# Performance work log

Measured on AMD Instinct MI355X. Metric: run time of the kernel, lower is better.

## Reference

```python
import jax, jax.numpy as jnp
import numpy as np

B, S, H = 2, 2048, 1024
NH, HD = 16, 64
EPS = 1e-12
SCALE = float(np.sqrt(HD))


def layer_norm(x, g, b, eps=EPS):
    m = jnp.mean(x, axis=-1, keepdims=True)
    v = jnp.mean(jnp.square(x - m), axis=-1, keepdims=True)
    return (x - m) * jax.lax.rsqrt(v + eps) * g + b


def setup_inputs() -> dict:
    key = jax.random.key(0)
    ks = jax.random.split(key, 12)
    std = 0.02 / np.sqrt(2 * 24)  # num_hidden_layers = 24
    return {
        "hidden_states": jax.random.normal(ks[0], (B, S, H), dtype=jnp.float32),
        "attention_mask": jnp.ones((B, S), dtype=jnp.float32),
        "Wq": jax.random.normal(ks[1], (H, H), dtype=jnp.float32) * std,
        "bq": jnp.zeros((H,), dtype=jnp.float32),
        "Wk": jax.random.normal(ks[2], (H, H), dtype=jnp.float32) * std,
        "bk": jnp.zeros((H,), dtype=jnp.float32),
        "Wv": jax.random.normal(ks[3], (H, H), dtype=jnp.float32) * std,
        "bv": jnp.zeros((H,), dtype=jnp.float32),
        "Wd": jax.random.normal(ks[4], (H, H), dtype=jnp.float32) * (1.0 / np.sqrt(H)),
        "bd": jnp.zeros((H,), dtype=jnp.float32),
        "ln_g": jnp.ones((H,), dtype=jnp.float32),
        "ln_b": jnp.zeros((H,), dtype=jnp.float32),
    }


def reference(hidden_states, attention_mask, Wq, bq, Wk, bk, Wv, bv, Wd, bd, ln_g, ln_b):
    x = hidden_states
    # NOTE: source computes pre_attention_norm(x) but the no-cache path uses raw x for Q/K/V.
    def heads(t):  # [B,S,H] -> [B,NH,S,HD]
        return t.reshape(B, S, NH, HD).transpose(0, 2, 1, 3)

    q = heads(x @ Wq.T + bq)
    k = heads(x @ Wk.T + bk)
    v = heads(x @ Wv.T + bv)

    scores = jnp.einsum("bhqd,bhkd->bhqk", q, k) / SCALE
    mask = (1.0 - attention_mask) * -10000.0  # [B,S] -> broadcast [B,1,1,S]
    scores = scores + mask[:, None, None, :]
    probs = jax.nn.softmax(scores.astype(jnp.float32), axis=-1).astype(x.dtype)

    ctx = jnp.einsum("bhqk,bhkd->bhqd", probs, v)
    ctx = ctx.transpose(0, 2, 1, 3).reshape(B, S, NH * HD)

    out = ctx @ Wd.T + bd
    out = layer_norm(out + x, ln_g, ln_b)
    out = jnp.where(jnp.isfinite(out), out, jnp.zeros_like(out))
    return out
```

## Files before the change

### kernel.cpp

```cpp
#include <hip/hip_runtime.h>
#include <cstdint>
#include <cstddef>

#define B_    2
#define S_    2048
#define H_    1024
#define NH_   16
#define HD_   64

typedef __attribute__((ext_vector_type(8))) __bf16 bf16x8;
typedef __attribute__((ext_vector_type(4))) __bf16 bf16x4;
typedef __attribute__((ext_vector_type(4))) float  f32x4;

typedef __attribute__((address_space(1))) const unsigned int gcu32_t;
typedef __attribute__((address_space(3))) unsigned int lu32_t;
#define GLOAD16(gp, lp) __builtin_amdgcn_global_load_lds((gcu32_t*)(gp), (lu32_t*)(lp), 16, 0, 0)

#if __has_builtin(__builtin_amdgcn_exp2f)
#define EXP2F(x) __builtin_amdgcn_exp2f(x)
#else
#define EXP2F(x) exp2f(x)
#endif

__device__ __forceinline__ short f2bf(float f) {
  union { float f; unsigned u; } v; v.f = f;
  unsigned r = v.u + 0x7fffu + ((v.u >> 16) & 1u);
  return (short)(r >> 16);
}

__global__ __launch_bounds__(256) void convert_kernel(
    const float* __restrict__ x,  const float* __restrict__ wq,
    const float* __restrict__ wk, const float* __restrict__ wv,
    const float* __restrict__ wd,
    short* __restrict__ xb,  short* __restrict__ wqb, short* __restrict__ wkb,
    short* __restrict__ wvb, short* __restrict__ wdb) {
  size_t i = ((size_t)blockIdx.x * 256 + threadIdx.x) * 4;
  const float* src; short* dst; size_t off;
  if      (i < 4194304u) { src = x;  dst = xb;  off = i; }
  else if (i < 5242880u) { src = wq; dst = wqb; off = i - 4194304u; }
  else if (i < 6291456u) { src = wk; dst = wkb; off = i - 5242880u; }
  else if (i < 7340032u) { src = wv; dst = wvb; off = i - 6291456u; }
  else                   { src = wd; dst = wdb; off = i - 7340032u; }
  float4 v = *(const float4*)(src + off);
  short4 o; o.x = f2bf(v.x); o.y = f2bf(v.y); o.z = f2bf(v.z); o.w = f2bf(v.w);
  *(short4*)(dst + off) = o;
}

template<int MODE>
__global__ __launch_bounds__(256, 2) void gemm_bt(
    const short* __restrict__ A,
    const short* __restrict__ Bq, const short* __restrict__ Bk,
    const short* __restrict__ Bv,
    const float* __restrict__ biasq, const float* __restrict__ biask,
    const float* __restrict__ biasv,
    short* __restrict__ outq, short* __restrict__ outk, short* __restrict__ outv,
    float* __restrict__ outy) {
  __shared__ short As[128 * 64];
  __shared__ short Bs[128 * 64];

  const short* Bw; const float* bias; short* outs = nullptr;
  if (MODE == 0) {
    int z = blockIdx.z;
    Bw   = (z == 0) ? Bq    : ((z == 1) ? Bk    : Bv);
    bias = (z == 0) ? biasq : ((z == 1) ? biask : biasv);
    outs = (z == 0) ? outq  : ((z == 1) ? outk  : outv);
  } else {
    Bw = Bq; bias = biasq;
  }

  const int K = 1024;
  int tid  = threadIdx.x;
  int lane = tid & 63, w = tid >> 6;
  int wr = w >> 1, wc = w & 1;
  int m0 = blockIdx.y * 128, n0 = blockIdx.x * 128;
  int l15 = lane & 15, lg = lane >> 4;

  int lr = lane >> 3, lc8 = 8 * ((lane & 7) ^ lr);
  const short* Ag = A  + (size_t)(m0 + w * 8 + lr) * K + lc8;
  const short* Bg = Bw + (size_t)(n0 + w * 8 + lr) * K + lc8;

  int cxor = (l15 & 7) * 8;

  f32x4 acc[4][4];
  for (int m = 0; m < 4; m++)
    for (int n = 0; n < 4; n++) acc[m][n] = {0.f, 0.f, 0.f, 0.f};

  for (int kt = 0; kt < 16; kt++) {
    __syncthreads();
    for (int it = 0; it < 4; it++) {
      GLOAD16(Ag + (size_t)it * 32 * K + kt * 64, &As[(w * 8 + it * 32) * 64]);
      GLOAD16(Bg + (size_t)it * 32 * K + kt * 64, &Bs[(w * 8 + it * 32) * 64]);
    }
    __syncthreads();
#pragma unroll
    for (int kkh = 0; kkh < 2; kkh++) {
      int col = (kkh * 32 + lg * 8) ^ cxor;
      bf16x8 af[4], bfr[4];
#pragma unroll
      for (int m = 0; m < 4; m++)
        af[m] = *(const bf16x8*)&As[(wr * 64 + m * 16 + l15) * 64 + col];
#pragma unroll
      for (int n = 0; n < 4; n++)
        bfr[n] = *(const bf16x8*)&Bs[(wc * 64 + n * 16 + l15) * 64 + col];
#pragma unroll
      for (int m = 0; m < 4; m++)
#pragma unroll
        for (int n = 0; n < 4; n++)
          acc[m][n] = __builtin_amdgcn_mfma_f32_16x16x32_bf16(af[m], bfr[n], acc[m][n], 0, 0, 0);
    }
  }

  for (int n = 0; n < 4; n++) {
    int col = n0 + wc * 64 + n * 16 + l15;
    float bval = bias[col];
    if (MODE == 0) {
      int h = col >> 6, d = col & 63;
      for (int m = 0; m < 4; m++) {
        int rowb = m0 + wr * 64 + m * 16 + lg * 4;
        for (int j = 0; j < 4; j++) {
          int row = rowb + j;
          int bb = row >> 11, s = row & 2047;
          outs[(((size_t)bb * NH_ + h) * S_ + s) * HD_ + d] = f2bf(acc[m][n][j] + bval);
        }
      }
    } else {
      for (int m = 0; m < 4; m++) {
        int rowb = m0 + wr * 64 + m * 16 + lg * 4;
        for (int j = 0; j < 4; j++)
          outy[(size_t)(rowb + j) * 1024 + col] = acc[m][n][j] + bval;
      }
    }
  }
}

__global__ __launch_bounds__(256, 2) void attn_kernel(
    const short* __restrict__ Q, const short* __restrict__ K,
    const short* __restrict__ V, const float* __restrict__ mask,
    short* __restrict__ ctx) {
  __shared__ short Qs[128 * 64];
  __shared__ short Ks[2][64 * 64];
  __shared__ short Vs[2][64 * 64];
  __shared__ short Ps[128 * 84];
  __shared__ float msk[2][64];

  int b = blockIdx.x;
  int bh = (b & 7) * 4 + ((b >> 3) >> 4);
  int qb = (b >> 3) & 15;
  int bidx = bh >> 4, h = bh & 15;
  int q0 = qb * 128;
  int tid = threadIdx.x, lane = tid & 63, w = tid >> 6;
  int l15 = lane & 15, lg = lane >> 4;

  const short* Qg = Q + (size_t)bh * S_ * HD_;
  const short* Kg = K + (size_t)bh * S_ * HD_;
  const short* Vg = V + (size_t)bh * S_ * HD_;

  int lr = lane >> 3, lc8 = 8 * ((lane & 7) ^ lr);
  int cxor = (l15 & 7) * 8;
  const float MLOG2E = -10000.0f * 1.442695041f;

  for (int it = 0; it < 4; it++) {
    int r = w * 8 + it * 32;
    GLOAD16(Qg + (size_t)(q0 + r + lr) * HD_ + lc8, &Qs[r * 64]);
  }
  for (int it = 0; it < 2; it++) {
    int r = w * 8 + it * 32;
    GLOAD16(Kg + (size_t)(r + lr) * HD_ + lc8, &Ks[0][r * 64]);
  }
  int vrow = tid >> 3, vcol = (tid & 7) * 8;
  int voff = ((vrow >> 2) * 4 + (vcol >> 4)) * 64 + (vrow & 3) * 16 + (vcol & 15);
  {
    int4 v0 = *(const int4*)&Vg[(size_t)vrow * HD_ + vcol];
    int4 v1 = *(const int4*)&Vg[(size_t)(vrow + 32) * HD_ + vcol];
    *(int4*)&Vs[0][voff] = v0;
    *(int4*)&Vs[0][voff + 2048] = v1;
  }
  if (tid < 64) msk[0][tid] = (1.0f - mask[bidx * S_ + tid]) * MLOG2E;
  __syncthreads();

  bf16x8 qreg[2][2];
#pragma unroll
  for (int kkh = 0; kkh < 2; kkh++)
#pragma unroll
    for (int m = 0; m < 2; m++) {
      int row = w * 32 + m * 16 + l15;
      qreg[kkh][m] = *(const bf16x8*)&Qs[row * 64 + ((kkh * 32 + lg * 8) ^ cxor)];
    }

  float mrun[2][4], lrun[2][4];
  f32x4 oacc[2][4];
#pragma unroll
  for (int m = 0; m < 2; m++)
#pragma unroll
    for (int j = 0; j < 4; j++) { mrun[m][j] = -1e30f; lrun[m][j] = 0.f; }
#pragma unroll
  for (int m = 0; m < 2; m++)
#pragma unroll
    for (int n = 0; n < 4; n++) oacc[m][n] = {0.f, 0.f, 0.f, 0.f};

  unsigned vtrbase = (unsigned)(uintptr_t)&Vs[0][0] + (unsigned)(lg * 1024 + l15 * 8);
  const float SC = 0.1803368977f;

  for (int kt = 0; kt < 32; kt++) {
    int cur = kt & 1;

    int4 vp0, vp1; float mp = 0.f;
    if (kt < 31) {
      const short* Kn = Kg + (size_t)(kt + 1) * 64 * HD_;
      for (int it = 0; it < 2; it++) {
        int r = w * 8 + it * 32;
        GLOAD16(Kn + (size_t)(r + lr) * HD_ + lc8, &Ks[cur ^ 1][r * 64]);
      }
      const short* Vn = Vg + (size_t)(kt + 1) * 64 * HD_;
      vp0 = *(const int4*)&Vn[(size_t)vrow * HD_ + vcol];
      vp1 = *(const int4*)&Vn[(size_t)(vrow + 32) * HD_ + vcol];
      if (tid < 64) mp = (1.0f - mask[bidx * S_ + (kt + 1) * 64 + tid]) * MLOG2E;
    }

    f32x4 sc[2][4];
#pragma unroll
    for (int m = 0; m < 2; m++)
#pragma unroll
      for (int n = 0; n < 4; n++) sc[m][n] = {0.f, 0.f, 0.f, 0.f};
#pragma unroll
    for (int kkh = 0; kkh < 2; kkh++) {
      int col = (kkh * 32 + lg * 8) ^ cxor;
      bf16x8 kb[4];
#pragma unroll
      for (int n = 0; n < 4; n++)
        kb[n] = *(const bf16x8*)&Ks[cur][(n * 16 + l15) * 64 + col];
#pragma unroll
      for (int m = 0; m < 2; m++)
#pragma unroll
        for (int n = 0; n < 4; n++)
          sc[m][n] = __builtin_amdgcn_mfma_f32_16x16x32_bf16(qreg[kkh][m], kb[n], sc[m][n], 0, 0, 0);
    }

    float mloc[4];
#pragma unroll
    for (int n = 0; n < 4; n++) mloc[n] = msk[cur][n * 16 + l15];

    float rmax[2][4];
#pragma unroll
    for (int m = 0; m < 2; m++)
#pragma unroll
      for (int j = 0; j < 4; j++) rmax[m][j] = -1e30f;
#pragma unroll
    for (int m = 0; m < 2; m++)
#pragma unroll
      for (int n = 0; n < 4; n++)
#pragma unroll
        for (int j = 0; j < 4; j++) {
          float t = sc[m][n][j] * SC + mloc[n];
          sc[m][n][j] = t;
          rmax[m][j] = fmaxf(rmax[m][j], t);
        }
    float alpha[2][4], rsum[2][4];
#pragma unroll
    for (int m = 0; m < 2; m++)
#pragma unroll
      for (int j = 0; j < 4; j++) {
        float t = rmax[m][j];
        for (int off = 1; off < 16; off <<= 1) t = fmaxf(t, __shfl_xor(t, off));
        float mn = fmaxf(mrun[m][j], t);
        alpha[m][j] = EXP2F(mrun[m][j] - mn);
        mrun[m][j] = mn;
        rsum[m][j] = 0.f;
      }
#pragma unroll
    for (int m = 0; m < 2; m++)
#pragma unroll
      for (int n = 0; n < 4; n++)
#pragma unroll
        for (int j = 0; j < 4; j++) {
          float p = EXP2F(sc[m][n][j] - mrun[m][j]);
          sc[m][n][j] = p;
          rsum[m][j] += p;
        }
#pragma unroll
    for (int m = 0; m < 2; m++)
#pragma unroll
      for (int j = 0; j < 4; j++) {
        float t = rsum[m][j];
        for (int off = 1; off < 16; off <<= 1) t += __shfl_xor(t, off);
        lrun[m][j] = lrun[m][j] * alpha[m][j] + t;
      }
#pragma unroll
    for (int m = 0; m < 2; m++)
#pragma unroll
      for (int n = 0; n < 4; n++)
#pragma unroll
        for (int j = 0; j < 4; j++) oacc[m][n][j] *= alpha[m][j];

#pragma unroll
    for (int m = 0; m < 2; m++)
#pragma unroll
      for (int n = 0; n < 4; n++)
#pragma unroll
        for (int j = 0; j < 4; j++)
          Ps[(w * 32 + m * 16 + lg * 4 + j) * 84 + n * 16 + l15] = f2bf(sc[m][n][j]);

    unsigned vtr = vtrbase + (unsigned)(cur * 8192);
#pragma unroll
    for (int kkh = 0; kkh < 2; kkh++) {
      bf16x4 vlo[4], vhi[4];
#pragma unroll
      for (int n = 0; n < 4; n++) {
        unsigned a = vtr + (unsigned)(kkh * 4096 + n * 128);
        asm volatile("ds_read_b64_tr_b16 %0, %2\n\t"
                     "ds_read_b64_tr_b16 %1, %2 offset:512"
                     : "=v"(vlo[n]), "=v"(vhi[n]) : "v"(a));
      }
      bf16x8 pa[2];
#pragma unroll
      for (int m = 0; m < 2; m++)
        pa[m] = *(const bf16x8*)&Ps[(w * 32 + m * 16 + l15) * 84 + kkh * 32 + lg * 8];
      asm volatile("s_waitcnt lgkmcnt(0)" ::: "memory");
      __builtin_amdgcn_sched_barrier(0);
#pragma unroll
      for (int n = 0; n < 4; n++) {
        bf16x8 vb = __builtin_shufflevector(vlo[n], vhi[n], 0, 1, 2, 3, 4, 5, 6, 7);
#pragma unroll
        for (int m = 0; m < 2; m++)
          oacc[m][n] = __builtin_amdgcn_mfma_f32_16x16x32_bf16(pa[m], vb, oacc[m][n], 0, 0, 0);
      }
    }

    if (kt < 31) {
      *(int4*)&Vs[cur ^ 1][voff] = vp0;
      *(int4*)&Vs[cur ^ 1][voff + 2048] = vp1;
      if (tid < 64) msk[cur ^ 1][tid] = mp;
    }
    __syncthreads();
  }

#pragma unroll
  for (int m = 0; m < 2; m++)
#pragma unroll
    for (int j = 0; j < 4; j++) {
      int sg = q0 + w * 32 + m * 16 + lg * 4 + j;
      float inv = 1.0f / lrun[m][j];
#pragma unroll
      for (int n = 0; n < 4; n++) {
        int d = n * 16 + l15;
        ctx[((size_t)(bidx * S_ + sg) * H_) + h * HD_ + d] = f2bf(oacc[m][n][j] * inv);
      }
    }
}

__global__ __launch_bounds__(256) void ln_kernel(
    const float* __restrict__ y, const float* __restrict__ x,
    const float* __restrict__ g, const float* __restrict__ bta,
    float* __restrict__ out) {
  __shared__ float red[4];
  int row = blockIdx.x;
  int tid = threadIdx.x, lane = tid & 63, w = tid >> 6;
  size_t base = (size_t)row * 1024 + tid * 4;
  float4 yv = *(const float4*)(y + base);
  float4 xv = *(const float4*)(x + base);
  float v0 = yv.x + xv.x, v1 = yv.y + xv.y, v2 = yv.z + xv.z, v3 = yv.w + xv.w;

  float ssum = v0 + v1 + v2 + v3;
  for (int off = 1; off < 64; off <<= 1) ssum += __shfl_xor(ssum, off);
  if (lane == 0) red[w] = ssum;
  __syncthreads();
  float mean = (red[0] + red[1] + red[2] + red[3]) * (1.f / 1024.f);
  __syncthreads();

  float d0 = v0 - mean, d1 = v1 - mean, d2 = v2 - mean, d3 = v3 - mean;
  float sq = d0 * d0 + d1 * d1 + d2 * d2 + d3 * d3;
  for (int off = 1; off < 64; off <<= 1) sq += __shfl_xor(sq, off);
  if (lane == 0) red[w] = sq;
  __syncthreads();
  float var = (red[0] + red[1] + red[2] + red[3]) * (1.f / 1024.f);
  float rs = 1.0f / sqrtf(var + 1e-12f);

  int c = tid * 4;
  float4 gv = *(const float4*)(g + c);
  float4 bv = *(const float4*)(bta + c);
  float o0 = d0 * rs * gv.x + bv.x;
  float o1 = d1 * rs * gv.y + bv.y;
  float o2 = d2 * rs * gv.z + bv.z;
  float o3 = d3 * rs * gv.w + bv.w;
  float4 ov;
  ov.x = __builtin_isfinite(o0) ? o0 : 0.f;
  ov.y = __builtin_isfinite(o1) ? o1 : 0.f;
  ov.z = __builtin_isfinite(o2) ? o2 : 0.f;
  ov.w = __builtin_isfinite(o3) ? o3 : 0.f;
  *(float4*)(out + base) = ov;
}

extern "C" void kernel_launch(void* const* d_in, const int* in_sizes, int n_in,
                              void* d_out, int out_size, void* d_ws, size_t ws_size,
                              hipStream_t stream) {
  (void)in_sizes; (void)n_in; (void)out_size; (void)ws_size;
  const float* x    = (const float*)d_in[0];
  const float* mask = (const float*)d_in[1];
  const float* Wq   = (const float*)d_in[2];
  const float* bq   = (const float*)d_in[3];
  const float* Wk   = (const float*)d_in[4];
  const float* bk   = (const float*)d_in[5];
  const float* Wv   = (const float*)d_in[6];
  const float* bv   = (const float*)d_in[7];
  const float* Wd   = (const float*)d_in[8];
  const float* bd   = (const float*)d_in[9];
  const float* ln_g = (const float*)d_in[10];
  const float* ln_b = (const float*)d_in[11];
  float* out = (float*)d_out;

  char* ws = (char*)d_ws;
  short* xb   = (short*)(ws);
  short* wqb  = (short*)(ws + ( 8ull << 20));
  short* wkb  = (short*)(ws + (10ull << 20));
  short* wvb  = (short*)(ws + (12ull << 20));
  short* wdb  = (short*)(ws + (14ull << 20));
  short* qb   = (short*)(ws + (16ull << 20));
  short* kb   = (short*)(ws + (24ull << 20));
  short* vb   = (short*)(ws + (32ull << 20));
  short* ctxb = (short*)(ws + (40ull << 20));
  float* y    = (float*)(ws + (48ull << 20));

  convert_kernel<<<8192, 256, 0, stream>>>(x, Wq, Wk, Wv, Wd, xb, wqb, wkb, wvb, wdb);
  gemm_bt<0><<<dim3(8, 32, 3), 256, 0, stream>>>(xb, wqb, wkb, wvb, bq, bk, bv,
                                                 qb, kb, vb, nullptr);
  attn_kernel<<<512, 256, 0, stream>>>(qb, kb, vb, mask, ctxb);
  gemm_bt<1><<<dim3(8, 32, 1), 256, 0, stream>>>(ctxb, wdb, nullptr, nullptr, bd,
                                                 nullptr, nullptr, nullptr, nullptr,
                                                 nullptr, y);
  ln_kernel<<<4096, 256, 0, stream>>>(y, x, ln_g, ln_b, out);
}
```

Measured before the change: 261.3 us.

## Transpose attention MFMAs, fold softmax scale into Q, add lazy rescale

The attention kernel now computes S^T = K·Q^T and O^T = V^T·P^T, so each lane holds a single query row. Row max and sum then need only two cross-lane shuffles, and P can be stored packed with v_cvt_pk_bf16_f32. The online-softmax rescale is skipped unless the running max rises by more than 8 (log2 units), and the softmax scale is folded into the Q projection epilogue. P reuses the Q shared buffer to cut LDS use, s_setprio wraps the MFMA sections, and GEMM occupancy is raised to 3; the lazy rescale risks larger fp32 intermediate values.

```diff
diff --git a/kernel.cpp b/kernel.cpp
--- a/kernel.cpp
+++ b/kernel.cpp
@@ -11,6 +11,7 @@
 typedef __attribute__((ext_vector_type(8))) __bf16 bf16x8;
 typedef __attribute__((ext_vector_type(4))) __bf16 bf16x4;
 typedef __attribute__((ext_vector_type(4))) float  f32x4;
+typedef __attribute__((ext_vector_type(2))) unsigned u32x2;
 
 typedef __attribute__((address_space(1))) const unsigned int gcu32_t;
 typedef __attribute__((address_space(3))) unsigned int lu32_t;
@@ -21,6 +22,8 @@
 #else
 #define EXP2F(x) exp2f(x)
 #endif
+
+#define SC_Q 0.1803368977f
 
 __device__ __forceinline__ short f2bf(float f) {
   union { float f; unsigned u; } v; v.f = f;
@@ -47,7 +50,7 @@
 }
 
 template<int MODE>
-__global__ __launch_bounds__(256, 2) void gemm_bt(
+__global__ __launch_bounds__(256, 3) void gemm_bt(
     const short* __restrict__ A,
     const short* __restrict__ Bq, const short* __restrict__ Bk,
     const short* __restrict__ Bv,
@@ -59,11 +62,13 @@
   __shared__ short Bs[128 * 64];
 
   const short* Bw; const float* bias; short* outs = nullptr;
+  float qscale = 1.0f;
   if (MODE == 0) {
     int z = blockIdx.z;
     Bw   = (z == 0) ? Bq    : ((z == 1) ? Bk    : Bv);
     bias = (z == 0) ? biasq : ((z == 1) ? biask : biasv);
     outs = (z == 0) ? outq  : ((z == 1) ? outk  : outv);
+    if (z == 0) qscale = SC_Q;
   } else {
     Bw = Bq; bias = biasq;
   }
@@ -92,6 +97,7 @@
       GLOAD16(Bg + (size_t)it * 32 * K + kt * 64, &Bs[(w * 8 + it * 32) * 64]);
     }
     __syncthreads();
+    __builtin_amdgcn_s_setprio(1);
 #pragma unroll
     for (int kkh = 0; kkh < 2; kkh++) {
       int col = (kkh * 32 + lg * 8) ^ cxor;
@@ -108,6 +114,7 @@
         for (int n = 0; n < 4; n++)
           acc[m][n] = __builtin_amdgcn_mfma_f32_16x16x32_bf16(af[m], bfr[n], acc[m][n], 0, 0, 0);
     }
+    __builtin_amdgcn_s_setprio(0);
   }
 
   for (int n = 0; n < 4; n++) {
@@ -120,7 +127,7 @@
         for (int j = 0; j < 4; j++) {
           int row = rowb + j;
           int bb = row >> 11, s = row & 2047;
-          outs[(((size_t)bb * NH_ + h) * S_ + s) * HD_ + d] = f2bf(acc[m][n][j] + bval);
+          outs[(((size_t)bb * NH_ + h) * S_ + s) * HD_ + d] = f2bf((acc[m][n][j] + bval) * qscale);
         }
       }
     } else {
@@ -137,10 +144,9 @@
     const short* __restrict__ Q, const short* __restrict__ K,
     const short* __restrict__ V, const float* __restrict__ mask,
     short* __restrict__ ctx) {
-  __shared__ short Qs[128 * 64];
+  __shared__ short QPs[128 * 72];
   __shared__ short Ks[2][64 * 64];
   __shared__ short Vs[2][64 * 64];
-  __shared__ short Ps[128 * 84];
   __shared__ float msk[2][64];
 
   int b = blockIdx.x;
@@ -161,7 +167,7 @@
 
   for (int it = 0; it < 4; it++) {
     int r = w * 8 + it * 32;
-    GLOAD16(Qg + (size_t)(q0 + r + lr) * HD_ + lc8, &Qs[r * 64]);
+    GLOAD16(Qg + (size_t)(q0 + r + lr) * HD_ + lc8, &QPs[r * 64]);
   }
   for (int it = 0; it < 2; it++) {
     int r = w * 8 + it * 32;
@@ -182,24 +188,22 @@
 #pragma unroll
   for (int kkh = 0; kkh < 2; kkh++)
 #pragma unroll
-    for (int m = 0; m < 2; m++) {
-      int row = w * 32 + m * 16 + l15;
-      qreg[kkh][m] = *(const bf16x8*)&Qs[row * 64 + ((kkh * 32 + lg * 8) ^ cxor)];
-    }
-
-  float mrun[2][4], lrun[2][4];
-  f32x4 oacc[2][4];
-#pragma unroll
-  for (int m = 0; m < 2; m++)
-#pragma unroll
-    for (int j = 0; j < 4; j++) { mrun[m][j] = -1e30f; lrun[m][j] = 0.f; }
-#pragma unroll
-  for (int m = 0; m < 2; m++)
-#pragma unroll
-    for (int n = 0; n < 4; n++) oacc[m][n] = {0.f, 0.f, 0.f, 0.f};
+    for (int qt = 0; qt < 2; qt++) {
+      int row = w * 32 + qt * 16 + l15;
+      qreg[kkh][qt] = *(const bf16x8*)&QPs[row * 64 + ((kkh * 32 + lg * 8) ^ cxor)];
+    }
+  __syncthreads();
+
+  float mrun[2] = {-1e30f, -1e30f};
+  float lrun[2] = {0.f, 0.f};
+  f32x4 oacc[4][2];
+#pragma unroll
+  for (int dt = 0; dt < 4; dt++)
+#pragma unroll
+    for (int qt = 0; qt < 2; qt++) oacc[dt][qt] = {0.f, 0.f, 0.f, 0.f};
 
   unsigned vtrbase = (unsigned)(uintptr_t)&Vs[0][0] + (unsigned)(lg * 1024 + l15 * 8);
-  const float SC = 0.1803368977f;
+  int psrow = (w * 32 + l15) * 72;
 
   for (int kt = 0; kt < 32; kt++) {
     int cur = kt & 1;
@@ -217,11 +221,12 @@
       if (tid < 64) mp = (1.0f - mask[bidx * S_ + (kt + 1) * 64 + tid]) * MLOG2E;
     }
 
-    f32x4 sc[2][4];
-#pragma unroll
-    for (int m = 0; m < 2; m++)
-#pragma unroll
-      for (int n = 0; n < 4; n++) sc[m][n] = {0.f, 0.f, 0.f, 0.f};
+    f32x4 sc[4][2];
+#pragma unroll
+    for (int n = 0; n < 4; n++)
+#pragma unroll
+      for (int qt = 0; qt < 2; qt++) sc[n][qt] = {0.f, 0.f, 0.f, 0.f};
+    __builtin_amdgcn_s_setprio(1);
 #pragma unroll
     for (int kkh = 0; kkh < 2; kkh++) {
       int col = (kkh * 32 + lg * 8) ^ cxor;
@@ -230,100 +235,108 @@
       for (int n = 0; n < 4; n++)
         kb[n] = *(const bf16x8*)&Ks[cur][(n * 16 + l15) * 64 + col];
 #pragma unroll
-      for (int m = 0; m < 2; m++)
-#pragma unroll
-        for (int n = 0; n < 4; n++)
-          sc[m][n] = __builtin_amdgcn_mfma_f32_16x16x32_bf16(qreg[kkh][m], kb[n], sc[m][n], 0, 0, 0);
-    }
-
-    float mloc[4];
-#pragma unroll
-    for (int n = 0; n < 4; n++) mloc[n] = msk[cur][n * 16 + l15];
-
-    float rmax[2][4];
-#pragma unroll
-    for (int m = 0; m < 2; m++)
-#pragma unroll
-      for (int j = 0; j < 4; j++) rmax[m][j] = -1e30f;
-#pragma unroll
-    for (int m = 0; m < 2; m++)
-#pragma unroll
       for (int n = 0; n < 4; n++)
 #pragma unroll
+        for (int qt = 0; qt < 2; qt++)
+          sc[n][qt] = __builtin_amdgcn_mfma_f32_16x16x32_bf16(kb[n], qreg[kkh][qt], sc[n][qt], 0, 0, 0);
+    }
+    __builtin_amdgcn_s_setprio(0);
+
+    f32x4 mv[4];
+#pragma unroll
+    for (int n = 0; n < 4; n++)
+      mv[n] = *(const f32x4*)&msk[cur][n * 16 + lg * 4];
+    float rmax[2];
+#pragma unroll
+    for (int qt = 0; qt < 2; qt++) {
+      float pm[4];
+#pragma unroll
+      for (int n = 0; n < 4; n++) {
+        float t0 = sc[n][qt][0] + mv[n][0];
+        float t1 = sc[n][qt][1] + mv[n][1];
+        float t2 = sc[n][qt][2] + mv[n][2];
+        float t3 = sc[n][qt][3] + mv[n][3];
+        sc[n][qt][0] = t0; sc[n][qt][1] = t1; sc[n][qt][2] = t2; sc[n][qt][3] = t3;
+        pm[n] = fmaxf(fmaxf(t0, t1), fmaxf(t2, t3));
+      }
+      float t = fmaxf(fmaxf(pm[0], pm[1]), fmaxf(pm[2], pm[3]));
+      t = fmaxf(t, __shfl_xor(t, 16));
+      t = fmaxf(t, __shfl_xor(t, 32));
+      rmax[qt] = t;
+    }
+
+    int need = (rmax[0] > mrun[0] + 8.f) || (rmax[1] > mrun[1] + 8.f);
+    if (__any(need)) {
+#pragma unroll
+      for (int qt = 0; qt < 2; qt++) {
+        float mn = fmaxf(mrun[qt], rmax[qt]);
+        float a = EXP2F(mrun[qt] - mn);
+        lrun[qt] *= a;
+        mrun[qt] = mn;
+#pragma unroll
+        for (int dt = 0; dt < 4; dt++)
+#pragma unroll
+          for (int j = 0; j < 4; j++) oacc[dt][qt][j] *= a;
+      }
+    }
+
+    float rsum[2] = {0.f, 0.f};
+#pragma unroll
+    for (int n = 0; n < 4; n++)
+#pragma unroll
+      for (int qt = 0; qt < 2; qt++)
+#pragma unroll
         for (int j = 0; j < 4; j++) {
-          float t = sc[m][n][j] * SC + mloc[n];
-          sc[m][n][j] = t;
-          rmax[m][j] = fmaxf(rmax[m][j], t);
+          float p = EXP2F(sc[n][qt][j] - mrun[qt]);
+          sc[n][qt][j] = p;
+          rsum[qt] += p;
         }
-    float alpha[2][4], rsum[2][4];
-#pragma unroll
-    for (int m = 0; m < 2; m++)
-#pragma unroll
-      for (int j = 0; j < 4; j++) {
-        float t = rmax[m][j];
-        for (int off = 1; off < 16; off <<= 1) t = fmaxf(t, __shfl_xor(t, off));
-        float mn = fmaxf(mrun[m][j], t);
-        alpha[m][j] = EXP2F(mrun[m][j] - mn);
-        mrun[m][j] = mn;
-        rsum[m][j] = 0.f;
-      }
-#pragma unroll
-    for (int m = 0; m < 2; m++)
-#pragma unroll
-      for (int n = 0; n < 4; n++)
-#pragma unroll
-        for (int j = 0; j < 4; j++) {
-          float p = EXP2F(sc[m][n][j] - mrun[m][j]);
-          sc[m][n][j] = p;
-          rsum[m][j] += p;
-        }
-#pragma unroll
-    for (int m = 0; m < 2; m++)
-#pragma unroll
-      for (int j = 0; j < 4; j++) {
-        float t = rsum[m][j];
-        for (int off = 1; off < 16; off <<= 1) t += __shfl_xor(t, off);
-        lrun[m][j] = lrun[m][j] * alpha[m][j] + t;
-      }
-#pragma unroll
-    for (int m = 0; m < 2; m++)
-#pragma unroll
-      for (int n = 0; n < 4; n++)
-#pragma unroll
-        for (int j = 0; j < 4; j++) oacc[m][n][j] *= alpha[m][j];
-
-#pragma unroll
-    for (int m = 0; m < 2; m++)
-#pragma unroll
-      for (int n = 0; n < 4; n++)
-#pragma unroll
-        for (int j = 0; j < 4; j++)
-          Ps[(w * 32 + m * 16 + lg * 4 + j) * 84 + n * 16 + l15] = f2bf(sc[m][n][j]);
+
+#pragma unroll
+    for (int qt = 0; qt < 2; qt++)
+#pragma unroll
+      for (int n = 0; n < 4; n++) {
+        unsigned pk0, pk1;
+        asm("v_cvt_pk_bf16_f32 %0, %1, %2" : "=v"(pk0) : "v"(sc[n][qt][0]), "v"(sc[n][qt][1]));
+        asm("v_cvt_pk_bf16_f32 %0, %1, %2" : "=v"(pk1) : "v"(sc[n][qt][2]), "v"(sc[n][qt][3]));
+        u32x2 wv2; wv2[0] = pk0; wv2[1] = pk1;
+        *(u32x2*)&QPs[psrow + qt * 16 * 72 + n * 16 + lg * 4] = wv2;
+      }
+
+#pragma unroll
+    for (int qt = 0; qt < 2; qt++) {
+      float t = rsum[qt];
+      t += __shfl_xor(t, 16);
+      t += __shfl_xor(t, 32);
+      lrun[qt] += t;
+    }
 
     unsigned vtr = vtrbase + (unsigned)(cur * 8192);
 #pragma unroll
-    for (int kkh = 0; kkh < 2; kkh++) {
+    for (int kb = 0; kb < 2; kb++) {
       bf16x4 vlo[4], vhi[4];
 #pragma unroll
-      for (int n = 0; n < 4; n++) {
-        unsigned a = vtr + (unsigned)(kkh * 4096 + n * 128);
+      for (int dt = 0; dt < 4; dt++) {
+        unsigned a = vtr + (unsigned)(kb * 4096 + dt * 128);
         asm volatile("ds_read_b64_tr_b16 %0, %2\n\t"
                      "ds_read_b64_tr_b16 %1, %2 offset:512"
-                     : "=v"(vlo[n]), "=v"(vhi[n]) : "v"(a));
-      }
-      bf16x8 pa[2];
-#pragma unroll
-      for (int m = 0; m < 2; m++)
-        pa[m] = *(const bf16x8*)&Ps[(w * 32 + m * 16 + l15) * 84 + kkh * 32 + lg * 8];
+                     : "=v"(vlo[dt]), "=v"(vhi[dt]) : "v"(a));
+      }
+      bf16x8 pb[2];
+#pragma unroll
+      for (int qt = 0; qt < 2; qt++)
+        pb[qt] = *(const bf16x8*)&QPs[psrow + qt * 16 * 72 + kb * 32 + lg * 8];
       asm volatile("s_waitcnt lgkmcnt(0)" ::: "memory");
       __builtin_amdgcn_sched_barrier(0);
-#pragma unroll
-      for (int n = 0; n < 4; n++) {
-        bf16x8 vb = __builtin_shufflevector(vlo[n], vhi[n], 0, 1, 2, 3, 4, 5, 6, 7);
-#pragma unroll
-        for (int m = 0; m < 2; m++)
-          oacc[m][n] = __builtin_amdgcn_mfma_f32_16x16x32_bf16(pa[m], vb, oacc[m][n], 0, 0, 0);
-      }
+      __builtin_amdgcn_s_setprio(1);
+#pragma unroll
+      for (int dt = 0; dt < 4; dt++) {
+        bf16x8 vb = __builtin_shufflevector(vlo[dt], vhi[dt], 0, 1, 2, 3, 4, 5, 6, 7);
+#pragma unroll
+        for (int qt = 0; qt < 2; qt++)
+          oacc[dt][qt] = __builtin_amdgcn_mfma_f32_16x16x32_bf16(vb, pb[qt], oacc[dt][qt], 0, 0, 0);
+      }
+      __builtin_amdgcn_s_setprio(0);
     }
 
     if (kt < 31) {
@@ -335,17 +348,20 @@
   }
 
 #pragma unroll
-  for (int m = 0; m < 2; m++)
-#pragma unroll
-    for (int j = 0; j < 4; j++) {
-      int sg = q0 + w * 32 + m * 16 + lg * 4 + j;
-      float inv = 1.0f / lrun[m][j];
-#pragma unroll
-      for (int n = 0; n < 4; n++) {
-        int d = n * 16 + l15;
-        ctx[((size_t)(bidx * S_ + sg) * H_) + h * HD_ + d] = f2bf(oacc[m][n][j] * inv);
-      }
-    }
+  for (int qt = 0; qt < 2; qt++) {
+    float inv = 1.0f / lrun[qt];
+    int sg = q0 + w * 32 + qt * 16 + l15;
+    size_t rowbase = ((size_t)(bidx * S_ + sg)) * H_ + h * HD_;
+#pragma unroll
+    for (int dt = 0; dt < 4; dt++) {
+      short4 st;
+      st.x = f2bf(oacc[dt][qt][0] * inv);
+      st.y = f2bf(oacc[dt][qt][1] * inv);
+      st.z = f2bf(oacc[dt][qt][2] * inv);
+      st.w = f2bf(oacc[dt][qt][3] * inv);
+      *(short4*)&ctx[rowbase + dt * 16 + lg * 4] = st;
+    }
+  }
 }
 
 __global__ __launch_bounds__(256) void ln_kernel(
```

Result: faster. 222.3 us (-14.9%).
